# Optimization experiments

Measured on AMD Instinct MI355X. Metric: run time of the kernel, lower is better.

The kernel has to match this reference:

```python
import jax, jax.numpy as jnp
import numpy as np

B, L, D, H = 4, 2048, 1024, 16
HD = D // H


def setup_inputs() -> dict:
    key = jax.random.key(0)
    k1, k2, k3 = jax.random.split(key, 3)
    # xavier_uniform bounds for Linear(d, 3d) and Linear(d, d)
    b_qkv = float(np.sqrt(6.0 / (D + 3 * D)))
    b_out = float(np.sqrt(6.0 / (D + D)))
    x = jax.random.normal(k1, (B, L, D), dtype=jnp.float32)
    W_qkv = jax.random.uniform(k2, (3 * D, D), dtype=jnp.float32, minval=-b_qkv, maxval=b_qkv)
    W_out = jax.random.uniform(k3, (D, D), dtype=jnp.float32, minval=-b_out, maxval=b_out)
    return {"x": x, "W_qkv": W_qkv, "W_out": W_out}


def reference(x, W_qkv, W_out):
    b, l, d = x.shape
    # fused QKV projection: [B,L,3d] -> [3,B,H,L,Hd]
    qkv = (x @ W_qkv.T).reshape(b, l, 3, H, HD).transpose(2, 0, 3, 1, 4)
    q, k, v = qkv[0], qkv[1], qkv[2]
    # naive causal attention: full [B,H,L,L] score matrix, as in the original
    scores = jnp.einsum('bhqd,bhkd->bhqk', q, k) / (HD ** 0.5)
    mask = jnp.tril(jnp.ones((l, l), dtype=bool))  # causal mask recomputed per call
    scores = jnp.where(mask, scores, -jnp.inf)
    attn = jax.nn.softmax(scores, axis=-1)
    ctx = jnp.einsum('bhqk,bhkd->bhqd', attn, v)          # [B,H,L,Hd]
    ctx = ctx.transpose(0, 2, 1, 3).reshape(b, l, d)       # [B,L,d]
    return ctx @ W_out.T
```

## Files before the change

### kernel.cpp

```cpp
#include <hip/hip_runtime.h>

#define BB 4
#define LL 2048
#define DD 1024
#define HH 16
#define HD 64

typedef __attribute__((ext_vector_type(8))) short s16x8;
typedef __attribute__((ext_vector_type(4))) short s16x4;
typedef __attribute__((ext_vector_type(4))) float f32x4;

#define SCALE_LOG2E 0.18033688011112042f

__device__ __forceinline__ short f2bf(float f) {
  union { float f; unsigned u; } c;
  c.f = f;
  return (short)((c.u + 0x7fffu + ((c.u >> 16) & 1u)) >> 16);
}

__device__ __forceinline__ void cp16(const void* g, void* l) {
  __builtin_amdgcn_global_load_lds(
      (const __attribute__((address_space(1))) void*)g,
      (__attribute__((address_space(3))) void*)l, 16, 0, 0);
}

__global__ __launch_bounds__(256) void f2b_kernel(const float* __restrict__ in,
                                                  short* __restrict__ out, int n4) {
  int i = blockIdx.x * blockDim.x + threadIdx.x;
  if (i >= n4) return;
  float4 v = ((const float4*)in)[i];
  s16x4 o;
  o[0] = f2bf(v.x);
  o[1] = f2bf(v.y);
  o[2] = f2bf(v.z);
  o[3] = f2bf(v.w);
  ((s16x4*)out)[i] = o;
}

template <int MODE>
__global__ __launch_bounds__(256) void gemm_bt(const short* __restrict__ A,
                                               const short* __restrict__ Bm,
                                               int K, int N,
                                               short* __restrict__ qo,
                                               short* __restrict__ ko,
                                               short* __restrict__ vo,
                                               float* __restrict__ fo) {
  __shared__ __align__(16) short As[4][128 * 32];
  __shared__ __align__(16) short Bs[4][128 * 32];
  const int tid = threadIdx.x;
  const int m0 = blockIdx.y * 128, n0 = blockIdx.x * 128;
  const int wave = tid >> 6, lane = tid & 63;
  const int quad = lane >> 4, c16 = lane & 15;
  const int wr = (wave >> 1) * 64, wc = (wave & 1) * 64;

  f32x4 zero = {0.f, 0.f, 0.f, 0.f};
  f32x4 acc[4][4];
#pragma unroll
  for (int i = 0; i < 4; i++)
#pragma unroll
    for (int j = 0; j < 4; j++) acc[i][j] = zero;

  const int row1 = tid >> 2;
  const int gsw = ((tid & 3) ^ ((tid >> 3) & 3)) * 8;
  const short* Ag = A + (size_t)(m0 + row1) * K + gsw;
  const short* Bg = Bm + (size_t)(n0 + row1) * K + gsw;
  const int rsw = (quad ^ ((c16 >> 1) & 3)) * 8;

  auto stage = [&](int t) {
    const int bi = t & 3, k0 = t << 5;
    cp16(Ag + k0, As[bi] + wave * 512);
    cp16(Ag + (size_t)64 * K + k0, As[bi] + 2048 + wave * 512);
    cp16(Bg + k0, Bs[bi] + wave * 512);
    cp16(Bg + (size_t)64 * K + k0, Bs[bi] + 2048 + wave * 512);
  };

  const int T = K >> 5;
  stage(0);
  stage(1);
  stage(2);
  asm volatile("s_waitcnt vmcnt(8)" ::: "memory");
  __builtin_amdgcn_s_barrier();
  asm volatile("" ::: "memory");

  for (int t = 0; t < T; t++) {
    const short* Asb = As[t & 3];
    const short* Bsb = Bs[t & 3];
    s16x8 af[4], bfv[4];
#pragma unroll
    for (int i = 0; i < 4; i++)
      af[i] = *(const s16x8*)&Asb[(wr + i * 16 + c16) * 32 + rsw];
#pragma unroll
    for (int j = 0; j < 4; j++)
      bfv[j] = *(const s16x8*)&Bsb[(wc + j * 16 + c16) * 32 + rsw];
    if (t + 3 < T) stage(t + 3);
    __builtin_amdgcn_s_setprio(1);
#pragma unroll
    for (int i = 0; i < 4; i++)
#pragma unroll
      for (int j = 0; j < 4; j++)
        acc[i][j] = __builtin_amdgcn_mfma_f32_16x16x32_bf16(af[i], bfv[j], acc[i][j], 0, 0, 0);
    __builtin_amdgcn_s_setprio(0);
    if (t < T - 3) asm volatile("s_waitcnt vmcnt(8)" ::: "memory");
    else if (t == T - 3) asm volatile("s_waitcnt vmcnt(4)" ::: "memory");
    else if (t == T - 2) asm volatile("s_waitcnt vmcnt(0)" ::: "memory");
    __builtin_amdgcn_s_barrier();
    asm volatile("" ::: "memory");
  }

  if (MODE == 0) {
#pragma unroll
    for (int j = 0; j < 4; j++) {
      const int gn = n0 + wc + j * 16 + c16;
      const int which = gn >> 10;
      const int h = (gn >> 6) & 15;
      const int hd = gn & 63;
      if (which == 2) {
#pragma unroll
        for (int i = 0; i < 4; i++) {
          const int gm = m0 + wr + i * 16 + quad * 4;
          const int b = gm >> 11, l = gm & 2047;
          s16x4 vv;
#pragma unroll
          for (int r = 0; r < 4; r++) vv[r] = f2bf(acc[i][j][r]);
          *(s16x4*)&vo[((size_t)((b << 4) + h) * HD + hd) * LL + l] = vv;
        }
      } else {
        short* dst = which == 0 ? qo : ko;
        const float sc = which == 0 ? SCALE_LOG2E : 1.0f;
#pragma unroll
        for (int i = 0; i < 4; i++)
#pragma unroll
          for (int r = 0; r < 4; r++) {
            const int gm = m0 + wr + i * 16 + quad * 4 + r;
            const int b = gm >> 11, l = gm & 2047;
            dst[((size_t)((b << 4) + h) * LL + l) * HD + hd] = f2bf(acc[i][j][r] * sc);
          }
      }
    }
  } else {
#pragma unroll
    for (int i = 0; i < 4; i++)
#pragma unroll
      for (int r = 0; r < 4; r++) {
        const int gm = m0 + wr + i * 16 + quad * 4 + r;
#pragma unroll
        for (int j = 0; j < 4; j++) {
          const int gn = n0 + wc + j * 16 + c16;
          fo[(size_t)gm * N + gn] = acc[i][j][r];
        }
      }
  }
}

__global__ __launch_bounds__(512, 4) void attn_kernel(const short* __restrict__ Qb,
                                                      const short* __restrict__ Kb,
                                                      const short* __restrict__ Vtb,
                                                      short* __restrict__ Cb) {
  const int pi = blockIdx.x;
  const int bh = blockIdx.y;
  const int tid = threadIdx.x;
  const int wave = tid >> 6, lane = tid & 63;
  const int quad = lane >> 4, c16 = lane & 15;
  const int sw = c16 & 7;
  const size_t base = (size_t)bh * LL * HD;
  const short* Q = Qb + base;
  const short* K = Kb + base;
  const short* Vt = Vtb + base;

  __shared__ __align__(16) short Ks[2][128 * 64];
  __shared__ __align__(16) short Vs[2][64 * 128];

  const f32x4 zero = {0.f, 0.f, 0.f, 0.f};
  const s16x4 ones = {(short)0x3F80, (short)0x3F80, (short)0x3F80, (short)0x3F80};

  const int k_r = lane >> 3, k_c = lane & 7;
  const int v_r = lane >> 4, v_c = lane & 15;
  const int ksw = (k_c ^ k_r) * 8;
  const int vsw = (v_c ^ ((wave * 4 + v_r) & 15)) * 8;
  auto stage = [&](int kb, int bi) {
#pragma unroll
    for (int i = 0; i < 2; i++) {
      const int gk = i * 64 + wave * 8 + k_r;
      cp16(K + (size_t)(kb + gk) * HD + ksw, &Ks[bi][(i * 64 + wave * 8) * 64]);
      const int gv = i * 32 + wave * 4 + v_r;
      cp16(Vt + (size_t)gv * LL + kb + vsw, &Vs[bi][(i * 32 + wave * 4) * 128]);
    }
  };

  auto pack4 = [&](const float* p) {
    union { float f; unsigned u; } a0, a1, a2, a3;
    a0.f = p[0]; a1.f = p[1]; a2.f = p[2]; a3.f = p[3];
    union { s16x4 v; unsigned u[2]; } r;
    r.u[0] = __builtin_amdgcn_perm(a1.u, a0.u, 0x07060302u);
    r.u[1] = __builtin_amdgcn_perm(a3.u, a2.u, 0x07060302u);
    return r.v;
  };

  for (int phase = 0; phase < 2; phase++) {
    const int qg = phase == 0 ? (15 - pi) : pi;
    const int qw = qg * 128 + wave * 16;
    const int tiles = qg + 1;

    s16x8 qf[2];
#pragma unroll
    for (int s = 0; s < 2; s++)
      qf[s] = *(const s16x8*)(Q + (size_t)(qw + c16) * HD + s * 32 + quad * 8);

    f32x4 o[4];
#pragma unroll
    for (int j4 = 0; j4 < 4; j4++) o[j4] = zero;
    f32x4 ol = zero;

    stage(0, 0);
    __syncthreads();

    for (int t = 0; t < tiles; t++) {
      const int kb = t * 128;
      if (t + 1 < tiles) stage(kb + 128, (t + 1) & 1);
      const short* Kt = &Ks[t & 1][0];
      const short* Vv = &Vs[t & 1][0];

      const int D = qw - kb;
      const int jm = min((D >> 4) + 1, 8);
      const int jb = D >> 4;

#pragma unroll
      for (int j = 0; j < 8; j++) {
        if (j >= jm) continue;
        s16x8 kf0 = *(const s16x8*)&Kt[(j * 16 + c16) * 64 + ((quad ^ sw) * 8)];
        s16x8 kf1 = *(const s16x8*)&Kt[(j * 16 + c16) * 64 + (((4 + quad) ^ sw) * 8)];
        s16x4 va[4];
#pragma unroll
        for (int j4 = 0; j4 < 4; j4++)
          va[j4] = *(const s16x4*)&Vv[(j4 * 16 + c16) * 128 +
                                      (((2 * j + (quad >> 1)) ^ c16) * 8) + (quad & 1) * 4];
        f32x4 s = __builtin_amdgcn_mfma_f32_16x16x32_bf16(kf0, qf[0], zero, 0, 0, 0);
        s = __builtin_amdgcn_mfma_f32_16x16x32_bf16(kf1, qf[1], s, 0, 0, 0);
        float p[4];
#pragma unroll
        for (int r = 0; r < 4; r++) p[r] = __builtin_amdgcn_exp2f(s[r]);
        if (j == jb) {
          const int thr = c16 + D - j * 16 - quad * 4;
#pragma unroll
          for (int r = 0; r < 4; r++)
            if (r > thr) p[r] = 0.f;
        }
        s16x4 pb = pack4(p);
        ol = __builtin_amdgcn_mfma_f32_16x16x16bf16_1k(ones, pb, ol, 0, 0, 0);
#pragma unroll
        for (int j4 = 0; j4 < 4; j4++)
          o[j4] = __builtin_amdgcn_mfma_f32_16x16x16bf16_1k(va[j4], pb, o[j4], 0, 0, 0);
      }

      __syncthreads();
    }

    const int b = bh >> 4, h2 = bh & 15;
    const float inv = 1.0f / ol[0];
    const int q = qw + c16;
#pragma unroll
    for (int j4 = 0; j4 < 4; j4++) {
      s16x4 ov;
#pragma unroll
      for (int r = 0; r < 4; r++) ov[r] = f2bf(o[j4][r] * inv);
      *(s16x4*)&Cb[(size_t)(b * LL + q) * DD + h2 * HD + j4 * 16 + quad * 4] = ov;
    }
  }
}

extern "C" void kernel_launch(void* const* d_in, const int* in_sizes, int n_in,
                              void* d_out, int out_size, void* d_ws, size_t ws_size,
                              hipStream_t stream) {
  const float* x = (const float*)d_in[0];
  const float* wqkv = (const float*)d_in[1];
  const float* wout = (const float*)d_in[2];
  float* out = (float*)d_out;

  const size_t NX = (size_t)BB * LL * DD;
  short* xb = (short*)d_ws;
  short* wqkvb = xb + NX;
  short* woutb = wqkvb + (size_t)3 * DD * DD;
  short* qb = woutb + (size_t)DD * DD;
  short* kb = qb + NX;
  short* vb = kb + NX;
  short* cb = vb + NX;

  f2b_kernel<<<dim3((unsigned)(NX / 4 / 256)), 256, 0, stream>>>(x, xb, (int)(NX / 4));
  f2b_kernel<<<dim3(3 * DD * DD / 4 / 256), 256, 0, stream>>>(wqkv, wqkvb, 3 * DD * DD / 4);
  f2b_kernel<<<dim3(DD * DD / 4 / 256), 256, 0, stream>>>(wout, woutb, DD * DD / 4);

  gemm_bt<0><<<dim3(3 * DD / 128, BB * LL / 128), 256, 0, stream>>>(
      xb, wqkvb, DD, 3 * DD, qb, kb, vb, nullptr);
  attn_kernel<<<dim3(8, BB * HH), 512, 0, stream>>>(qb, kb, vb, cb);
  gemm_bt<1><<<dim3(DD / 128, BB * LL / 128), 256, 0, stream>>>(
      cb, woutb, DD, DD, nullptr, nullptr, nullptr, out);
}
```

Baseline: 250.8 us.

## Merge fp32-to-bf16 conversions into one launch and cut GEMM pipeline to three stages

The three separate fp32-to-bf16 conversion launches become a single kernel that picks its source and destination by block index, which saves launch overhead. The GEMM's LDS ring buffer shrinks from four stages to three, with prefetch distance two and matching vmcnt waits, and launch_bounds now requests three blocks per CU. The intent is to cut LDS use per block (from 64KB to 48KB) so more blocks fit per CU and overlap better. The trade-off is a shallower prefetch depth, which could expose global-load latency.

```diff
diff --git a/kernel.cpp b/kernel.cpp
--- a/kernel.cpp
+++ b/kernel.cpp
@@ -24,10 +24,24 @@
       (__attribute__((address_space(3))) void*)l, 16, 0, 0);
 }
 
-__global__ __launch_bounds__(256) void f2b_kernel(const float* __restrict__ in,
-                                                  short* __restrict__ out, int n4) {
-  int i = blockIdx.x * blockDim.x + threadIdx.x;
-  if (i >= n4) return;
+__global__ __launch_bounds__(256) void f2b_all(const float* __restrict__ x,
+                                               const float* __restrict__ wqkv,
+                                               const float* __restrict__ wout,
+                                               short* __restrict__ xb,
+                                               short* __restrict__ wqkvb,
+                                               short* __restrict__ woutb) {
+  const int bid = blockIdx.x;
+  const float* in;
+  short* out;
+  int i0;
+  if (bid < 8192) {
+    in = x; out = xb; i0 = bid;
+  } else if (bid < 8192 + 3072) {
+    in = wqkv; out = wqkvb; i0 = bid - 8192;
+  } else {
+    in = wout; out = woutb; i0 = bid - (8192 + 3072);
+  }
+  const int i = i0 * 256 + threadIdx.x;
   float4 v = ((const float4*)in)[i];
   s16x4 o;
   o[0] = f2bf(v.x);
@@ -38,15 +52,15 @@
 }
 
 template <int MODE>
-__global__ __launch_bounds__(256) void gemm_bt(const short* __restrict__ A,
-                                               const short* __restrict__ Bm,
-                                               int K, int N,
-                                               short* __restrict__ qo,
-                                               short* __restrict__ ko,
-                                               short* __restrict__ vo,
-                                               float* __restrict__ fo) {
-  __shared__ __align__(16) short As[4][128 * 32];
-  __shared__ __align__(16) short Bs[4][128 * 32];
+__global__ __launch_bounds__(256, 3) void gemm_bt(const short* __restrict__ A,
+                                                  const short* __restrict__ Bm,
+                                                  int K, int N,
+                                                  short* __restrict__ qo,
+                                                  short* __restrict__ ko,
+                                                  short* __restrict__ vo,
+                                                  float* __restrict__ fo) {
+  __shared__ __align__(16) short As[3][128 * 32];
+  __shared__ __align__(16) short Bs[3][128 * 32];
   const int tid = threadIdx.x;
   const int m0 = blockIdx.y * 128, n0 = blockIdx.x * 128;
   const int wave = tid >> 6, lane = tid & 63;
@@ -66,8 +80,8 @@
   const short* Bg = Bm + (size_t)(n0 + row1) * K + gsw;
   const int rsw = (quad ^ ((c16 >> 1) & 3)) * 8;
 
-  auto stage = [&](int t) {
-    const int bi = t & 3, k0 = t << 5;
+  auto stage = [&](int t, int bi) {
+    const int k0 = t << 5;
     cp16(Ag + k0, As[bi] + wave * 512);
     cp16(Ag + (size_t)64 * K + k0, As[bi] + 2048 + wave * 512);
     cp16(Bg + k0, Bs[bi] + wave * 512);
@@ -75,16 +89,16 @@
   };
 
   const int T = K >> 5;
-  stage(0);
-  stage(1);
-  stage(2);
-  asm volatile("s_waitcnt vmcnt(8)" ::: "memory");
+  stage(0, 0);
+  stage(1, 1);
+  asm volatile("s_waitcnt vmcnt(4)" ::: "memory");
   __builtin_amdgcn_s_barrier();
   asm volatile("" ::: "memory");
 
+  int bcur = 0;
   for (int t = 0; t < T; t++) {
-    const short* Asb = As[t & 3];
-    const short* Bsb = Bs[t & 3];
+    const short* Asb = As[bcur];
+    const short* Bsb = Bs[bcur];
     s16x8 af[4], bfv[4];
 #pragma unroll
     for (int i = 0; i < 4; i++)
@@ -92,7 +106,11 @@
 #pragma unroll
     for (int j = 0; j < 4; j++)
       bfv[j] = *(const s16x8*)&Bsb[(wc + j * 16 + c16) * 32 + rsw];
-    if (t + 3 < T) stage(t + 3);
+    if (t + 2 < T) {
+      int b2 = bcur + 2;
+      if (b2 >= 3) b2 -= 3;
+      stage(t + 2, b2);
+    }
     __builtin_amdgcn_s_setprio(1);
 #pragma unroll
     for (int i = 0; i < 4; i++)
@@ -100,11 +118,11 @@
       for (int j = 0; j < 4; j++)
         acc[i][j] = __builtin_amdgcn_mfma_f32_16x16x32_bf16(af[i], bfv[j], acc[i][j], 0, 0, 0);
     __builtin_amdgcn_s_setprio(0);
-    if (t < T - 3) asm volatile("s_waitcnt vmcnt(8)" ::: "memory");
-    else if (t == T - 3) asm volatile("s_waitcnt vmcnt(4)" ::: "memory");
+    if (t < T - 2) asm volatile("s_waitcnt vmcnt(4)" ::: "memory");
     else if (t == T - 2) asm volatile("s_waitcnt vmcnt(0)" ::: "memory");
     __builtin_amdgcn_s_barrier();
     asm volatile("" ::: "memory");
+    bcur = (bcur == 2) ? 0 : bcur + 1;
   }
 
   if (MODE == 0) {
@@ -285,9 +303,7 @@
   short* vb = kb + NX;
   short* cb = vb + NX;
 
-  f2b_kernel<<<dim3((unsigned)(NX / 4 / 256)), 256, 0, stream>>>(x, xb, (int)(NX / 4));
-  f2b_kernel<<<dim3(3 * DD * DD / 4 / 256), 256, 0, stream>>>(wqkv, wqkvb, 3 * DD * DD / 4);
-  f2b_kernel<<<dim3(DD * DD / 4 / 256), 256, 0, stream>>>(wout, woutb, DD * DD / 4);
+  f2b_all<<<dim3(8192 + 3072 + 1024), 256, 0, stream>>>(x, wqkv, wout, xb, wqkvb, woutb);
 
   gemm_bt<0><<<dim3(3 * DD / 128, BB * LL / 128), 256, 0, stream>>>(
       xb, wqkvb, DD, 3 * DD, qb, kb, vb, nullptr);
```

New measurement: 239.9 us. 1.05x faster.
